# Kernel optimization log

Measured on AMD Instinct MI355X. Metric: run time of the kernel, lower is better.

The kernel has to match this reference:

```python
import jax, jax.numpy as jnp
import numpy as np


def setup_inputs() -> dict:
    key = jax.random.key(0)
    ks = jax.random.split(key, 6)
    S, B, E = 2048, 2, 1024
    scale = 1.0 / np.sqrt(E)
    return {
        "query": jax.random.normal(ks[0], (S, B, E), dtype=jnp.float32),
        "key": jax.random.normal(ks[1], (S, B, E), dtype=jnp.float32),
        "value": jax.random.normal(ks[2], (S, B, E), dtype=jnp.float32),
        "in_proj_w": jax.random.normal(ks[3], (3 * E, E), dtype=jnp.float32) * scale,
        "in_proj_b": jnp.zeros((3 * E,), dtype=jnp.float32),
        "out_proj_w": jax.random.normal(ks[4], (E, E), dtype=jnp.float32) * scale,
        "out_proj_b": jnp.zeros((E,), dtype=jnp.float32),
        "num_heads": 16,
        "block_size": 128,
    }


def reference(query, key, value, in_proj_w, in_proj_b, out_proj_w, out_proj_b,
              num_heads, block_size):
    # Shapes: query/key/value [S, B, E] (torch MHA default, batch_first=False)
    S, B, E = query.shape
    H = num_heads
    D = E // H

    wq, wk, wv = jnp.split(in_proj_w, 3, axis=0)   # each [E, E]
    bq, bk, bv = jnp.split(in_proj_b, 3, axis=0)   # each [E]

    def proj(x, w, b):
        # [S,B,E] @ [E,E]^T + b -> [B,H,S,D]
        y = x @ w.T + b
        return y.reshape(S, B, H, D).transpose(1, 2, 0, 3)

    q = proj(query, wq, bq) * (1.0 / np.sqrt(D))
    k = proj(key, wk, bk)
    v = proj(value, wv, bv)

    # Dense scores with banded mask: allowed iff i-block <= j <= i+block-1
    scores = jnp.einsum("bhsd,bhtd->bhst", q, k)  # [B,H,S,S]
    i = jnp.arange(S)[:, None]
    j = jnp.arange(S)[None, :]
    allowed = (j >= i - block_size) & (j < i + block_size)  # [S,S]
    neg_inf = jnp.asarray(-jnp.inf, dtype=scores.dtype)
    scores = jnp.where(allowed[None, None], scores, neg_inf)

    attn = jax.nn.softmax(scores, axis=-1)
    ctx = jnp.einsum("bhst,bhtd->bhsd", attn, v)           # [B,H,S,D]
    ctx = ctx.transpose(2, 0, 1, 3).reshape(S, B, E)       # [S,B,E]
    return ctx @ out_proj_w.T + out_proj_b
```

## Files before the change

### kernel.cpp

```cpp
#include <hip/hip_runtime.h>
#include <hip/hip_bf16.h>

#define S_LEN 2048
#define BATCH 2
#define EMB   1024
#define NHEAD 16
#define HDIM  64
#define WIN   128

typedef __attribute__((ext_vector_type(8))) short short8;
typedef __attribute__((ext_vector_type(4))) float floatx4;

__device__ __forceinline__ unsigned int pk2bf(float a, float b) {
    unsigned int ua = __builtin_bit_cast(unsigned int, a);
    unsigned int ub = __builtin_bit_cast(unsigned int, b);
    ua += 0x7fffu + ((ua >> 16) & 1u);
    ub += 0x7fffu + ((ub >> 16) & 1u);
    return (ua >> 16) | (ub & 0xffff0000u);
}
__device__ __forceinline__ unsigned short f2bf(float f) {
    unsigned int u = __builtin_bit_cast(unsigned int, f);
    u += 0x7fffu + ((u >> 16) & 1u);
    return (unsigned short)(u >> 16);
}

__device__ __forceinline__ void gl_lds16(const unsigned short* g, unsigned short* l) {
    __builtin_amdgcn_global_load_lds(
        (const __attribute__((address_space(1))) unsigned int*)g,
        (__attribute__((address_space(3))) unsigned int*)l,
        16, 0, 0);
}

#define QKV_UNITS 524288
#define WI_UNITS  393216
#define WO_UNITS  131072

__global__ __launch_bounds__(256)
void convert_kernel(const float* __restrict__ xq, const float* __restrict__ xk,
                    const float* __restrict__ xv, const float* __restrict__ wi,
                    const float* __restrict__ wo,
                    unsigned short* __restrict__ xqb, unsigned short* __restrict__ xkb,
                    unsigned short* __restrict__ xvb, unsigned short* __restrict__ wib,
                    unsigned short* __restrict__ wob)
{
    const size_t u = (size_t)blockIdx.x * 256 + threadIdx.x;
    const float* src;
    unsigned short* dst;
    size_t off;
    if (u < 3 * (size_t)QKV_UNITS) {
        const int which = (int)(u / QKV_UNITS);
        off = (u % QKV_UNITS) * 8;
        src = (which == 0) ? xq : (which == 1) ? xk : xv;
        dst = (which == 0) ? xqb : (which == 1) ? xkb : xvb;
    } else if (u < 3 * (size_t)QKV_UNITS + WI_UNITS) {
        off = (u - 3 * (size_t)QKV_UNITS) * 8;
        src = wi; dst = wib;
    } else {
        off = (u - (3 * (size_t)QKV_UNITS + WI_UNITS)) * 8;
        src = wo; dst = wob;
    }
    float4 a = *reinterpret_cast<const float4*>(src + off);
    float4 b = *reinterpret_cast<const float4*>(src + off + 4);
    uint4 p = {pk2bf(a.x, a.y), pk2bf(a.z, a.w), pk2bf(b.x, b.y), pk2bf(b.z, b.w)};
    *reinterpret_cast<uint4*>(dst + off) = p;
}

__global__ __launch_bounds__(256)
void qkv_gemm_kernel(const unsigned short* __restrict__ xqb,
                     const unsigned short* __restrict__ xkb,
                     const unsigned short* __restrict__ xvb,
                     const unsigned short* __restrict__ wib,
                     const float* __restrict__ bias,
                     unsigned short* __restrict__ qo,
                     unsigned short* __restrict__ ko,
                     unsigned short* __restrict__ vto)
{
    __shared__ unsigned short As[128 * 64];
    __shared__ unsigned short Bs[128 * 64];

    const int bid  = blockIdx.x;
    const int which = bid >> 8;
    const int bx   = (bid >> 5) & 7;
    const int by   = bid & 31;

    const unsigned short* A = (which == 0) ? xqb : (which == 1) ? xkb : xvb;
    const unsigned short* W = wib + (size_t)which * EMB * EMB;
    const float* bv = bias + which * EMB;
    const float scale = (which == 0) ? 0.125f : 1.0f;

    const int tid  = threadIdx.x;
    const int lane = tid & 63;
    const int wave = tid >> 6;
    const int quad = lane >> 4;
    const int c16  = lane & 15;
    const int wm   = (wave & 1) << 6;
    const int wn   = (wave >> 1) << 6;

    const int rowBase = by * 128;
    const int colBase = bx * 128;

    const int lrow = lane >> 3;
    const int lseg = (((lane & 7) ^ lrow) << 3);

    floatx4 acc[4][4];
    #pragma unroll
    for (int i = 0; i < 4; ++i)
        #pragma unroll
        for (int j = 0; j < 4; ++j)
            acc[i][j] = (floatx4){0.f, 0.f, 0.f, 0.f};

    const int rxor = c16 & 7;

    for (int k0 = 0; k0 < EMB; k0 += 64) {
        __syncthreads();
        #pragma unroll
        for (int t = 0; t < 4; ++t) {
            const int c = wave * 4 + t;
            const int row = c * 8 + lrow;
            gl_lds16(A + (size_t)(rowBase + row) * EMB + k0 + lseg, &As[c * 512]);
            gl_lds16(W + (size_t)(colBase + row) * EMB + k0 + lseg, &Bs[c * 512]);
        }
        __syncthreads();

        #pragma unroll
        for (int kk = 0; kk < 2; ++kk) {
            const int soff = (((quad + 4 * kk) ^ rxor) << 3);
            short8 af[4], bf[4];
            #pragma unroll
            for (int mi = 0; mi < 4; ++mi)
                af[mi] = *reinterpret_cast<const short8*>(
                    &As[(wm + mi * 16 + c16) * 64 + soff]);
            #pragma unroll
            for (int ni = 0; ni < 4; ++ni)
                bf[ni] = *reinterpret_cast<const short8*>(
                    &Bs[(wn + ni * 16 + c16) * 64 + soff]);

            #pragma unroll
            for (int mi = 0; mi < 4; ++mi)
                #pragma unroll
                for (int ni = 0; ni < 4; ++ni)
                    acc[mi][ni] = __builtin_amdgcn_mfma_f32_16x16x32_bf16(
                        af[mi], bf[ni], acc[mi][ni], 0, 0, 0);
        }
    }

    if (which != 2) {
        #pragma unroll
        for (int ni = 0; ni < 4; ++ni) {
            const int n_full = colBase + wn + ni * 16 + c16;
            const float bb = bv[n_full];
            const int h = n_full >> 6;
            const int d = n_full & 63;
            #pragma unroll
            for (int mi = 0; mi < 4; ++mi) {
                #pragma unroll
                for (int r = 0; r < 4; ++r) {
                    const int m_g = rowBase + wm + mi * 16 + quad * 4 + r;
                    const int s   = m_g >> 1;
                    const int b   = m_g & 1;
                    const int bh  = b * NHEAD + h;
                    const unsigned short val = f2bf((acc[mi][ni][r] + bb) * scale);
                    if (which == 0)
                        qo[((size_t)bh * S_LEN + s) * HDIM + d] = val;
                    else
                        ko[((size_t)bh * S_LEN + s) * HDIM + d] = val;
                }
            }
        }
    } else {
        __syncthreads();
        unsigned short* Ts = (wn == 0) ? As : Bs;
        #pragma unroll
        for (int ni = 0; ni < 4; ++ni) {
            const int n_loc2 = ni * 16 + c16;
            const int n_full = colBase + wn + n_loc2;
            const float bb = bv[n_full];
            const int k2 = (n_loc2 & 3) << 4;
            #pragma unroll
            for (int mi = 0; mi < 4; ++mi) {
                #pragma unroll
                for (int r = 0; r < 4; ++r) {
                    const int m_local = wm + mi * 16 + quad * 4 + r;
                    const int lin = (m_local & 1) * 64 + (m_local >> 1);
                    Ts[n_loc2 * 128 + (lin ^ k2)] = f2bf(acc[mi][ni][r] + bb);
                }
            }
        }
        __syncthreads();
        const int nl = tid & 127;
        const int b  = tid >> 7;
        const int n_loc2 = nl & 63;
        const unsigned short* Tsrc = (nl < 64) ? As : Bs;
        const int k2 = (n_loc2 & 3) << 4;
        const int n_full = colBase + nl;
        const int h = n_full >> 6;
        const int d = n_full & 63;
        const int bh = b * NHEAD + h;
        unsigned short* dst = vto + ((size_t)bh * HDIM + d) * S_LEN + (rowBase >> 1);
        #pragma unroll
        for (int g = 0; g < 8; ++g) {
            const uint4 vv = *reinterpret_cast<const uint4*>(
                &Tsrc[n_loc2 * 128 + ((b * 64 + g * 8) ^ k2)]);
            *reinterpret_cast<uint4*>(dst + g * 8) = vv;
        }
    }
}

#define AT_STRIDE 72

__global__ __launch_bounds__(256)
void attn_mfma_kernel(const unsigned short* __restrict__ q,
                      const unsigned short* __restrict__ k,
                      const unsigned short* __restrict__ vt,
                      unsigned short* __restrict__ ctx)
{
    __shared__ unsigned short Qs[64 * AT_STRIDE];
    __shared__ unsigned short Ks[64 * AT_STRIDE];
    __shared__ unsigned short Vts[64 * AT_STRIDE];
    __shared__ unsigned short Ps[64 * AT_STRIDE];

    const int bid = blockIdx.x;
    const int bh  = bid & 31;
    const int s0  = (bid >> 5) * 64;
    const int tid = threadIdx.x;
    const int lane = tid & 63;
    const int wave = tid >> 6;
    const int quad = lane >> 4;
    const int c16  = lane & 15;

    const size_t base_qk = ((size_t)bh * S_LEN) * HDIM;
    const size_t base_vt = ((size_t)bh * HDIM) * S_LEN;

    const int srow = tid >> 2;
    const int sseg = (tid & 3) << 4;
    {
        const unsigned short* src = q + base_qk + (size_t)(s0 + srow) * HDIM + sseg;
        uint4 v0 = *reinterpret_cast<const uint4*>(src);
        uint4 v1 = *reinterpret_cast<const uint4*>(src + 8);
        *reinterpret_cast<uint4*>(&Qs[srow * AT_STRIDE + sseg])     = v0;
        *reinterpret_cast<uint4*>(&Qs[srow * AT_STRIDE + sseg + 8]) = v1;
    }

    float m_[4], l_[4];
    floatx4 ob[4];
    #pragma unroll
    for (int r = 0; r < 4; ++r) { m_[r] = -1.0e30f; l_[r] = 0.f; }
    #pragma unroll
    for (int dt = 0; dt < 4; ++dt) ob[dt] = (floatx4){0.f, 0.f, 0.f, 0.f};

    int c0 = s0 - 128; if (c0 < 0) c0 = 0;
    int c1 = s0 + 192; if (c1 > S_LEN) c1 = S_LEN;

    uint4 k0v, k1v, v0v, v1v;
#define LOADKV(CB)                                                                \
    {                                                                             \
        const unsigned short* ksrc = k + base_qk + (size_t)((CB) + srow) * HDIM + sseg; \
        const unsigned short* vsrc = vt + base_vt + (size_t)srow * S_LEN + (CB) + sseg; \
        k0v = *reinterpret_cast<const uint4*>(ksrc);                              \
        k1v = *reinterpret_cast<const uint4*>(ksrc + 8);                          \
        v0v = *reinterpret_cast<const uint4*>(vsrc);                              \
        v1v = *reinterpret_cast<const uint4*>(vsrc + 8);                          \
    }

    LOADKV(c0);

    for (int cb = c0; cb < c1; cb += 64) {
        __syncthreads();
        *reinterpret_cast<uint4*>(&Ks[srow * AT_STRIDE + sseg])      = k0v;
        *reinterpret_cast<uint4*>(&Ks[srow * AT_STRIDE + sseg + 8])  = k1v;
        *reinterpret_cast<uint4*>(&Vts[srow * AT_STRIDE + sseg])     = v0v;
        *reinterpret_cast<uint4*>(&Vts[srow * AT_STRIDE + sseg + 8]) = v1v;
        __syncthreads();
        if (cb + 64 < c1) LOADKV(cb + 64);

        floatx4 sc[4];
        #pragma unroll
        for (int jt = 0; jt < 4; ++jt) sc[jt] = (floatx4){0.f, 0.f, 0.f, 0.f};
        {
            short8 af0 = *reinterpret_cast<const short8*>(
                &Qs[(wave * 16 + c16) * AT_STRIDE + quad * 8]);
            short8 af1 = *reinterpret_cast<const short8*>(
                &Qs[(wave * 16 + c16) * AT_STRIDE + 32 + quad * 8]);
            #pragma unroll
            for (int jt = 0; jt < 4; ++jt) {
                short8 bf0 = *reinterpret_cast<const short8*>(
                    &Ks[(jt * 16 + c16) * AT_STRIDE + quad * 8]);
                short8 bf1 = *reinterpret_cast<const short8*>(
                    &Ks[(jt * 16 + c16) * AT_STRIDE + 32 + quad * 8]);
                sc[jt] = __builtin_amdgcn_mfma_f32_16x16x32_bf16(af0, bf0, sc[jt], 0, 0, 0);
                sc[jt] = __builtin_amdgcn_mfma_f32_16x16x32_bf16(af1, bf1, sc[jt], 0, 0, 0);
            }
        }

        #pragma unroll
        for (int r = 0; r < 4; ++r) {
            const int qg = s0 + wave * 16 + quad * 4 + r;
            float rm = -3.0e38f;
            #pragma unroll
            for (int jt = 0; jt < 4; ++jt) {
                const int jg = cb + jt * 16 + c16;
                float x = sc[jt][r];
                if (jg < qg - WIN || jg >= qg + WIN) x = -3.0e38f;
                sc[jt][r] = x;
                rm = fmaxf(rm, x);
            }
            rm = fmaxf(rm, __shfl_xor(rm, 1));
            rm = fmaxf(rm, __shfl_xor(rm, 2));
            rm = fmaxf(rm, __shfl_xor(rm, 4));
            rm = fmaxf(rm, __shfl_xor(rm, 8));
            const float mn    = fmaxf(m_[r], rm);
            const float alpha = __expf(m_[r] - mn);
            float rs = 0.f;
            #pragma unroll
            for (int jt = 0; jt < 4; ++jt) {
                const float p = __expf(sc[jt][r] - mn);
                sc[jt][r] = p;
                rs += p;
            }
            rs += __shfl_xor(rs, 1);
            rs += __shfl_xor(rs, 2);
            rs += __shfl_xor(rs, 4);
            rs += __shfl_xor(rs, 8);
            l_[r] = l_[r] * alpha + rs;
            m_[r] = mn;
            #pragma unroll
            for (int dt = 0; dt < 4; ++dt) ob[dt][r] *= alpha;
        }

        #pragma unroll
        for (int jt = 0; jt < 4; ++jt)
            #pragma unroll
            for (int r = 0; r < 4; ++r)
                Ps[(wave * 16 + quad * 4 + r) * AT_STRIDE + jt * 16 + c16] =
                    f2bf(sc[jt][r]);

        {
            short8 pa0 = *reinterpret_cast<const short8*>(
                &Ps[(wave * 16 + c16) * AT_STRIDE + quad * 8]);
            short8 pa1 = *reinterpret_cast<const short8*>(
                &Ps[(wave * 16 + c16) * AT_STRIDE + 32 + quad * 8]);
            #pragma unroll
            for (int dt = 0; dt < 4; ++dt) {
                short8 bv0 = *reinterpret_cast<const short8*>(
                    &Vts[(dt * 16 + c16) * AT_STRIDE + quad * 8]);
                short8 bv1 = *reinterpret_cast<const short8*>(
                    &Vts[(dt * 16 + c16) * AT_STRIDE + 32 + quad * 8]);
                ob[dt] = __builtin_amdgcn_mfma_f32_16x16x32_bf16(pa0, bv0, ob[dt], 0, 0, 0);
                ob[dt] = __builtin_amdgcn_mfma_f32_16x16x32_bf16(pa1, bv1, ob[dt], 0, 0, 0);
            }
        }
    }
#undef LOADKV

    const int b = bh >> 4;
    const int h = bh & 15;
    #pragma unroll
    for (int r = 0; r < 4; ++r) {
        const int sg  = s0 + wave * 16 + quad * 4 + r;
        const float inv = 1.0f / l_[r];
        #pragma unroll
        for (int dt = 0; dt < 4; ++dt) {
            const int d = dt * 16 + c16;
            ctx[((size_t)(sg * BATCH + b) << 10) + (h << 6) + d] = f2bf(ob[dt][r] * inv);
        }
    }
}

__global__ __launch_bounds__(256)
void out_gemm_kernel(const unsigned short* __restrict__ ctxb,
                     const unsigned short* __restrict__ wob,
                     const float* __restrict__ bias,
                     float* __restrict__ out)
{
    __shared__ unsigned short As[128 * 64];
    __shared__ unsigned short Bs[128 * 64];

    const int bid = blockIdx.x;
    const int bx  = bid >> 5;
    const int by  = bid & 31;

    const int tid  = threadIdx.x;
    const int lane = tid & 63;
    const int wave = tid >> 6;
    const int quad = lane >> 4;
    const int c16  = lane & 15;
    const int wm   = (wave & 1) << 6;
    const int wn   = (wave >> 1) << 6;

    const int rowBase = by * 128;
    const int colBase = bx * 128;

    const int lrow = lane >> 3;
    const int lseg = (((lane & 7) ^ lrow) << 3);

    floatx4 acc[4][4];
    #pragma unroll
    for (int i = 0; i < 4; ++i)
        #pragma unroll
        for (int j = 0; j < 4; ++j)
            acc[i][j] = (floatx4){0.f, 0.f, 0.f, 0.f};

    const int rxor = c16 & 7;

    for (int k0 = 0; k0 < EMB; k0 += 64) {
        __syncthreads();
        #pragma unroll
        for (int t = 0; t < 4; ++t) {
            const int c = wave * 4 + t;
            const int row = c * 8 + lrow;
            gl_lds16(ctxb + (size_t)(rowBase + row) * EMB + k0 + lseg, &As[c * 512]);
            gl_lds16(wob  + (size_t)(colBase + row) * EMB + k0 + lseg, &Bs[c * 512]);
        }
        __syncthreads();

        #pragma unroll
        for (int kk = 0; kk < 2; ++kk) {
            const int soff = (((quad + 4 * kk) ^ rxor) << 3);
            short8 af[4], bf[4];
            #pragma unroll
            for (int mi = 0; mi < 4; ++mi)
                af[mi] = *reinterpret_cast<const short8*>(
                    &As[(wm + mi * 16 + c16) * 64 + soff]);
            #pragma unroll
            for (int ni = 0; ni < 4; ++ni)
                bf[ni] = *reinterpret_cast<const short8*>(
                    &Bs[(wn + ni * 16 + c16) * 64 + soff]);

            #pragma unroll
            for (int mi = 0; mi < 4; ++mi)
                #pragma unroll
                for (int ni = 0; ni < 4; ++ni)
                    acc[mi][ni] = __builtin_amdgcn_mfma_f32_16x16x32_bf16(
                        af[mi], bf[ni], acc[mi][ni], 0, 0, 0);
        }
    }

    #pragma unroll
    for (int ni = 0; ni < 4; ++ni) {
        const int n_full = colBase + wn + ni * 16 + c16;
        const float bb = bias[n_full];
        #pragma unroll
        for (int mi = 0; mi < 4; ++mi) {
            #pragma unroll
            for (int r = 0; r < 4; ++r) {
                const int m_g = rowBase + wm + mi * 16 + quad * 4 + r;
                out[(size_t)m_g * EMB + n_full] = acc[mi][ni][r] + bb;
            }
        }
    }
}

extern "C" void kernel_launch(void* const* d_in, const int* in_sizes, int n_in,
                              void* d_out, int out_size, void* d_ws, size_t ws_size,
                              hipStream_t stream) {
    const float* query = (const float*)d_in[0];
    const float* key   = (const float*)d_in[1];
    const float* value = (const float*)d_in[2];
    const float* in_w  = (const float*)d_in[3];
    const float* in_b  = (const float*)d_in[4];
    const float* out_w = (const float*)d_in[5];
    const float* out_b = (const float*)d_in[6];

    const size_t PLANE = (size_t)BATCH * NHEAD * S_LEN * HDIM;
    unsigned short* xqb = (unsigned short*)d_ws;
    unsigned short* xkb = xqb + PLANE;
    unsigned short* xvb = xkb + PLANE;
    unsigned short* wib = xvb + PLANE;
    unsigned short* wob = wib + (size_t)3 * EMB * EMB;
    unsigned short* qo  = wob + (size_t)EMB * EMB;
    unsigned short* ko  = qo + PLANE;
    unsigned short* vto = ko + PLANE;
    unsigned short* cw  = vto + PLANE;

    convert_kernel<<<8192, 256, 0, stream>>>(query, key, value, in_w, out_w,
                                             xqb, xkb, xvb, wib, wob);

    qkv_gemm_kernel<<<768, 256, 0, stream>>>(xqb, xkb, xvb, wib, in_b, qo, ko, vto);

    attn_mfma_kernel<<<1024, 256, 0, stream>>>(qo, ko, vto, cw);

    out_gemm_kernel<<<256, 256, 0, stream>>>(cw, wob, out_b, (float*)d_out);
}
```

Measured before the change: 202.5 us.

## Halve QKV GEMM K-tile LDS and transpose score MFMA in attention

The QKV projection GEMM now stages 32-wide K slices instead of 64, halving shared memory per block (16KB instead of 32KB) so more blocks can be resident. The swizzle is adjusted to match, and the V-transpose epilogue is split into two passes that reuse the smaller buffer. In the attention kernel the QK^T MFMA operands are swapped so each lane holds one query row's scores. This cuts softmax reductions from per-row 4-step shuffles to 2 shuffles and allows packed P stores to LDS, at the cost of shuffles to redistribute alpha and l. Halving the K tile doubles the number of barriers and load phases in the GEMM loop.

```diff
diff --git a/kernel.cpp b/kernel.cpp
--- a/kernel.cpp
+++ b/kernel.cpp
@@ -75,8 +75,9 @@
                      unsigned short* __restrict__ ko,
                      unsigned short* __restrict__ vto)
 {
-    __shared__ unsigned short As[128 * 64];
-    __shared__ unsigned short Bs[128 * 64];
+    __shared__ unsigned short SM[8192];
+    unsigned short* As = SM;
+    unsigned short* Bs = SM + 4096;
 
     const int bid  = blockIdx.x;
     const int which = bid >> 8;
@@ -99,8 +100,8 @@
     const int rowBase = by * 128;
     const int colBase = bx * 128;
 
-    const int lrow = lane >> 3;
-    const int lseg = (((lane & 7) ^ lrow) << 3);
+    const int lrow = lane >> 2;
+    const int lseg = (((lane & 3) ^ (lrow & 3)) << 3);
 
     floatx4 acc[4][4];
     #pragma unroll
@@ -109,39 +110,36 @@
         for (int j = 0; j < 4; ++j)
             acc[i][j] = (floatx4){0.f, 0.f, 0.f, 0.f};
 
-    const int rxor = c16 & 7;
-
-    for (int k0 = 0; k0 < EMB; k0 += 64) {
-        __syncthreads();
-        #pragma unroll
-        for (int t = 0; t < 4; ++t) {
-            const int c = wave * 4 + t;
-            const int row = c * 8 + lrow;
+    const int rxor = c16 & 3;
+    const int soff = ((quad ^ rxor) << 3);
+
+    for (int k0 = 0; k0 < EMB; k0 += 32) {
+        __syncthreads();
+        #pragma unroll
+        for (int t = 0; t < 2; ++t) {
+            const int c = wave * 2 + t;
+            const int row = c * 16 + lrow;
             gl_lds16(A + (size_t)(rowBase + row) * EMB + k0 + lseg, &As[c * 512]);
             gl_lds16(W + (size_t)(colBase + row) * EMB + k0 + lseg, &Bs[c * 512]);
         }
         __syncthreads();
 
-        #pragma unroll
-        for (int kk = 0; kk < 2; ++kk) {
-            const int soff = (((quad + 4 * kk) ^ rxor) << 3);
-            short8 af[4], bf[4];
-            #pragma unroll
-            for (int mi = 0; mi < 4; ++mi)
-                af[mi] = *reinterpret_cast<const short8*>(
-                    &As[(wm + mi * 16 + c16) * 64 + soff]);
+        short8 af[4], bf[4];
+        #pragma unroll
+        for (int mi = 0; mi < 4; ++mi)
+            af[mi] = *reinterpret_cast<const short8*>(
+                &As[(wm + mi * 16 + c16) * 32 + soff]);
+        #pragma unroll
+        for (int ni = 0; ni < 4; ++ni)
+            bf[ni] = *reinterpret_cast<const short8*>(
+                &Bs[(wn + ni * 16 + c16) * 32 + soff]);
+
+        #pragma unroll
+        for (int mi = 0; mi < 4; ++mi)
             #pragma unroll
             for (int ni = 0; ni < 4; ++ni)
-                bf[ni] = *reinterpret_cast<const short8*>(
-                    &Bs[(wn + ni * 16 + c16) * 64 + soff]);
-
-            #pragma unroll
-            for (int mi = 0; mi < 4; ++mi)
-                #pragma unroll
-                for (int ni = 0; ni < 4; ++ni)
-                    acc[mi][ni] = __builtin_amdgcn_mfma_f32_16x16x32_bf16(
-                        af[mi], bf[ni], acc[mi][ni], 0, 0, 0);
-        }
+                acc[mi][ni] = __builtin_amdgcn_mfma_f32_16x16x32_bf16(
+                    af[mi], bf[ni], acc[mi][ni], 0, 0, 0);
     }
 
     if (which != 2) {
@@ -168,40 +166,43 @@
             }
         }
     } else {
-        __syncthreads();
-        unsigned short* Ts = (wn == 0) ? As : Bs;
-        #pragma unroll
-        for (int ni = 0; ni < 4; ++ni) {
-            const int n_loc2 = ni * 16 + c16;
-            const int n_full = colBase + wn + n_loc2;
-            const float bb = bv[n_full];
-            const int k2 = (n_loc2 & 3) << 4;
-            #pragma unroll
-            for (int mi = 0; mi < 4; ++mi) {
+        for (int p = 0; p < 2; ++p) {
+            __syncthreads();
+            if ((wn >> 6) == p) {
                 #pragma unroll
-                for (int r = 0; r < 4; ++r) {
-                    const int m_local = wm + mi * 16 + quad * 4 + r;
-                    const int lin = (m_local & 1) * 64 + (m_local >> 1);
-                    Ts[n_loc2 * 128 + (lin ^ k2)] = f2bf(acc[mi][ni][r] + bb);
+                for (int ni = 0; ni < 4; ++ni) {
+                    const int n_loc2 = ni * 16 + c16;
+                    const int n_full = colBase + p * 64 + n_loc2;
+                    const float bb = bv[n_full];
+                    const int k2 = (n_loc2 & 3) << 4;
+                    #pragma unroll
+                    for (int mi = 0; mi < 4; ++mi) {
+                        #pragma unroll
+                        for (int r = 0; r < 4; ++r) {
+                            const int m_local = wm + mi * 16 + quad * 4 + r;
+                            const int lin = (m_local & 1) * 64 + (m_local >> 1);
+                            SM[n_loc2 * 128 + (lin ^ k2)] = f2bf(acc[mi][ni][r] + bb);
+                        }
+                    }
                 }
             }
-        }
-        __syncthreads();
-        const int nl = tid & 127;
-        const int b  = tid >> 7;
-        const int n_loc2 = nl & 63;
-        const unsigned short* Tsrc = (nl < 64) ? As : Bs;
-        const int k2 = (n_loc2 & 3) << 4;
-        const int n_full = colBase + nl;
-        const int h = n_full >> 6;
-        const int d = n_full & 63;
-        const int bh = b * NHEAD + h;
-        unsigned short* dst = vto + ((size_t)bh * HDIM + d) * S_LEN + (rowBase >> 1);
-        #pragma unroll
-        for (int g = 0; g < 8; ++g) {
-            const uint4 vv = *reinterpret_cast<const uint4*>(
-                &Tsrc[n_loc2 * 128 + ((b * 64 + g * 8) ^ k2)]);
-            *reinterpret_cast<uint4*>(dst + g * 8) = vv;
+            __syncthreads();
+            const int nlp = tid & 63;
+            const int b   = (tid >> 6) & 1;
+            const int sh  = tid >> 7;
+            const int k2  = (nlp & 3) << 4;
+            const int n_full = colBase + p * 64 + nlp;
+            const int h = n_full >> 6;
+            const int d = n_full & 63;
+            const int bh = b * NHEAD + h;
+            unsigned short* dst = vto + ((size_t)bh * HDIM + d) * S_LEN
+                                      + (rowBase >> 1) + sh * 32;
+            #pragma unroll
+            for (int g = 0; g < 4; ++g) {
+                const uint4 vv = *reinterpret_cast<const uint4*>(
+                    &SM[nlp * 128 + ((b * 64 + sh * 32 + g * 8) ^ k2)]);
+                *reinterpret_cast<uint4*>(dst + g * 8) = vv;
+            }
         }
     }
 }
@@ -241,12 +242,12 @@
         *reinterpret_cast<uint4*>(&Qs[srow * AT_STRIDE + sseg + 8]) = v1;
     }
 
-    float m_[4], l_[4];
+    float m_ = -1.0e30f, l_ = 0.f;
     floatx4 ob[4];
     #pragma unroll
-    for (int r = 0; r < 4; ++r) { m_[r] = -1.0e30f; l_[r] = 0.f; }
-    #pragma unroll
     for (int dt = 0; dt < 4; ++dt) ob[dt] = (floatx4){0.f, 0.f, 0.f, 0.f};
+
+    const int qg = s0 + wave * 16 + c16;
 
     int c0 = s0 - 128; if (c0 < 0) c0 = 0;
     int c1 = s0 + 192; if (c1 > S_LEN) c1 = S_LEN;
@@ -287,52 +288,57 @@
                     &Ks[(jt * 16 + c16) * AT_STRIDE + quad * 8]);
                 short8 bf1 = *reinterpret_cast<const short8*>(
                     &Ks[(jt * 16 + c16) * AT_STRIDE + 32 + quad * 8]);
-                sc[jt] = __builtin_amdgcn_mfma_f32_16x16x32_bf16(af0, bf0, sc[jt], 0, 0, 0);
-                sc[jt] = __builtin_amdgcn_mfma_f32_16x16x32_bf16(af1, bf1, sc[jt], 0, 0, 0);
-            }
-        }
-
-        #pragma unroll
-        for (int r = 0; r < 4; ++r) {
-            const int qg = s0 + wave * 16 + quad * 4 + r;
-            float rm = -3.0e38f;
-            #pragma unroll
-            for (int jt = 0; jt < 4; ++jt) {
-                const int jg = cb + jt * 16 + c16;
+                sc[jt] = __builtin_amdgcn_mfma_f32_16x16x32_bf16(bf0, af0, sc[jt], 0, 0, 0);
+                sc[jt] = __builtin_amdgcn_mfma_f32_16x16x32_bf16(bf1, af1, sc[jt], 0, 0, 0);
+            }
+        }
+
+        float rm = -3.0e38f;
+        #pragma unroll
+        for (int jt = 0; jt < 4; ++jt) {
+            #pragma unroll
+            for (int r = 0; r < 4; ++r) {
+                const int jg = cb + jt * 16 + quad * 4 + r;
                 float x = sc[jt][r];
                 if (jg < qg - WIN || jg >= qg + WIN) x = -3.0e38f;
                 sc[jt][r] = x;
                 rm = fmaxf(rm, x);
             }
-            rm = fmaxf(rm, __shfl_xor(rm, 1));
-            rm = fmaxf(rm, __shfl_xor(rm, 2));
-            rm = fmaxf(rm, __shfl_xor(rm, 4));
-            rm = fmaxf(rm, __shfl_xor(rm, 8));
-            const float mn    = fmaxf(m_[r], rm);
-            const float alpha = __expf(m_[r] - mn);
-            float rs = 0.f;
-            #pragma unroll
-            for (int jt = 0; jt < 4; ++jt) {
+        }
+        rm = fmaxf(rm, __shfl_xor(rm, 16));
+        rm = fmaxf(rm, __shfl_xor(rm, 32));
+        const float mn    = fmaxf(m_, rm);
+        const float alpha = __expf(m_ - mn);
+        float rs = 0.f;
+        #pragma unroll
+        for (int jt = 0; jt < 4; ++jt) {
+            #pragma unroll
+            for (int r = 0; r < 4; ++r) {
                 const float p = __expf(sc[jt][r] - mn);
                 sc[jt][r] = p;
                 rs += p;
             }
-            rs += __shfl_xor(rs, 1);
-            rs += __shfl_xor(rs, 2);
-            rs += __shfl_xor(rs, 4);
-            rs += __shfl_xor(rs, 8);
-            l_[r] = l_[r] * alpha + rs;
-            m_[r] = mn;
-            #pragma unroll
-            for (int dt = 0; dt < 4; ++dt) ob[dt][r] *= alpha;
-        }
-
-        #pragma unroll
-        for (int jt = 0; jt < 4; ++jt)
-            #pragma unroll
-            for (int r = 0; r < 4; ++r)
-                Ps[(wave * 16 + quad * 4 + r) * AT_STRIDE + jt * 16 + c16] =
-                    f2bf(sc[jt][r]);
+        }
+        rs += __shfl_xor(rs, 16);
+        rs += __shfl_xor(rs, 32);
+        l_ = l_ * alpha + rs;
+        m_ = mn;
+
+        #pragma unroll
+        for (int r = 0; r < 4; ++r) {
+            const float ar = __shfl(alpha, (lane & 48) | (quad * 4 + r));
+            #pragma unroll
+            for (int dt = 0; dt < 4; ++dt) ob[dt][r] *= ar;
+        }
+
+        #pragma unroll
+        for (int jt = 0; jt < 4; ++jt) {
+            uint2 pw;
+            pw.x = pk2bf(sc[jt][0], sc[jt][1]);
+            pw.y = pk2bf(sc[jt][2], sc[jt][3]);
+            *reinterpret_cast<uint2*>(
+                &Ps[(wave * 16 + c16) * AT_STRIDE + jt * 16 + quad * 4]) = pw;
+        }
 
         {
             short8 pa0 = *reinterpret_cast<const short8*>(
@@ -357,7 +363,8 @@
     #pragma unroll
     for (int r = 0; r < 4; ++r) {
         const int sg  = s0 + wave * 16 + quad * 4 + r;
-        const float inv = 1.0f / l_[r];
+        const float lr = __shfl(l_, (lane & 48) | (quad * 4 + r));
+        const float inv = 1.0f / lr;
         #pragma unroll
         for (int dt = 0; dt < 4; ++dt) {
             const int d = dt * 16 + c16;
```

New measurement: 202.3 us. Within noise of the previous version (-0.1%).
